# Performance work log

Hardware: AMD Instinct MI355X
Metric: run time of the kernel (lower is better)

Reference implementation:

```python
import jax, jax.numpy as jnp
import numpy as np

N_HEAD = 16
ROPE_BASE = 10000.0


def _rope_tables(T, head_dim, dtype):
    inv_freq = 1.0 / (ROPE_BASE ** (jnp.arange(0, head_dim, 2, dtype=jnp.float32) / head_dim))
    t = jnp.arange(T, dtype=jnp.float32)
    freqs = t[:, None] * inv_freq[None, :]          # [T, hd/2]
    emb = jnp.concatenate([freqs, freqs], axis=-1)  # [T, hd]
    return jnp.cos(emb).astype(dtype), jnp.sin(emb).astype(dtype)


def _rotate_half(x):
    h = x.shape[-1] // 2
    return jnp.concatenate([-x[..., h:], x[..., :h]], axis=-1)


def setup_inputs() -> dict:
    key = jax.random.key(0)
    k1, k2, k3 = jax.random.split(key, 3)
    B, T, C = 2, 2048, 1024
    x = jax.random.normal(k1, (B, T, C), dtype=jnp.float32)
    w_attn = jax.random.normal(k2, (3 * C, C), dtype=jnp.float32) * (1.0 / np.sqrt(C))
    w_proj = jax.random.normal(k3, (C, C), dtype=jnp.float32) * (1.0 / np.sqrt(C))
    return {"x": x, "w_attn": w_attn, "w_proj": w_proj}


def reference(x, w_attn, w_proj):
    B, T, C = x.shape
    H = N_HEAD
    hd = C // H

    qkv = jnp.einsum('btc,fc->btf', x, w_attn)          # [B,T,3C]
    q, k, v = jnp.split(qkv, 3, axis=-1)
    # [B,H,T,hd]
    q = q.reshape(B, T, H, hd).transpose(0, 2, 1, 3)
    k = k.reshape(B, T, H, hd).transpose(0, 2, 1, 3)
    v = v.reshape(B, T, H, hd).transpose(0, 2, 1, 3)

    cos, sin = _rope_tables(T, hd, x.dtype)             # [T,hd]
    cos = cos[None, None]
    sin = sin[None, None]
    q = q * cos + _rotate_half(q) * sin
    k = k * cos + _rotate_half(k) * sin

    scale = 1.0 / np.sqrt(hd)
    scores = jnp.einsum('bhqd,bhkd->bhqk', q, k) * scale  # [B,H,T,T]
    causal = jnp.tril(jnp.ones((T, T), dtype=bool))
    scores = jnp.where(causal[None, None], scores, jnp.finfo(scores.dtype).min)
    attn = jax.nn.softmax(scores, axis=-1)
    out = jnp.einsum('bhqk,bhkd->bhqd', attn, v)          # [B,H,T,hd]
    out = out.transpose(0, 2, 1, 3).reshape(B, T, C)
    return jnp.einsum('btc,oc->bto', out, w_proj)
```

## Files before the change

### kernel.cpp

```cpp
#include <hip/hip_runtime.h>
#include <hip/hip_bf16.h>
#include <stdint.h>

typedef unsigned short u16;
typedef __bf16 bf16x8 __attribute__((ext_vector_type(8)));
typedef float f32x4 __attribute__((ext_vector_type(4)));

#define B_ 2
#define T_ 2048
#define C_ 1024
#define H_ 16
#define HD 64
#define M_ (B_ * T_)
#define N3 (3 * C_)

#define WAITV(N) asm volatile("s_waitcnt vmcnt(" #N ")" ::: "memory")

__device__ __forceinline__ float bf2f(u16 u) {
  return __uint_as_float(((unsigned int)u) << 16);
}
__device__ __forceinline__ u16 f2bf(float f) {
  unsigned int u = __float_as_uint(f);
  u += 0x7FFF + ((u >> 16) & 1);
  return (u16)(u >> 16);
}
__device__ __forceinline__ unsigned cvt_pk_bf16(float lo, float hi) {
  unsigned r;
  asm("v_cvt_pk_bf16_f32 %0, %1, %2" : "=v"(r) : "v"(lo), "v"(hi));
  return r;
}
__device__ __forceinline__ void async16(void* ldsp, const void* gp) {
  __builtin_amdgcn_global_load_lds(
      (const __attribute__((address_space(1))) unsigned int*)gp,
      (__attribute__((address_space(3))) unsigned int*)ldsp, 16, 0, 0);
}

union U16x8 { uint4 v; u16 u[8]; };

__device__ __forceinline__ bf16x8 ldsAfrag(const char* base, int row, int kbyte) {
  int off = (row * 128 + kbyte) ^ ((row & 7) << 4);
  uint4 t = *reinterpret_cast<const uint4*>(base + off);
  return __builtin_bit_cast(bf16x8, t);
}
__device__ __forceinline__ bf16x8 ldsRead(const char* p) {
  uint4 t = *reinterpret_cast<const uint4*>(p);
  return __builtin_bit_cast(bf16x8, t);
}

#define NX4  (M_ * C_ / 4)
#define NWA4 (N3 * C_ / 4)
#define NWP4 (C_ * C_ / 4)
#define NTOT4 (NX4 + NWA4 + NWP4)
__global__ void cvt3(const float* __restrict__ x, const float* __restrict__ wa,
                     const float* __restrict__ wp, u16* __restrict__ xb,
                     u16* __restrict__ wab, u16* __restrict__ wpb) {
  int i = blockIdx.x * blockDim.x + threadIdx.x;
  int stride = gridDim.x * blockDim.x;
  for (; i < NTOT4; i += stride) {
    const float* src; u16* dst; int j = i;
    if (j < NX4) { src = x; dst = xb; }
    else if (j < NX4 + NWA4) { j -= NX4; src = wa; dst = wab; }
    else { j -= NX4 + NWA4; src = wp; dst = wpb; }
    float4 v = reinterpret_cast<const float4*>(src)[j];
    uint2 o;
    o.x = (unsigned)f2bf(v.x) | ((unsigned)f2bf(v.y) << 16);
    o.y = (unsigned)f2bf(v.z) | ((unsigned)f2bf(v.w) << 16);
    reinterpret_cast<uint2*>(dst)[j] = o;
  }
}

__global__ void rope_tables_kernel(float2* __restrict__ rtab) {
  int t = blockIdx.x;
  int i = threadIdx.x;
  float inv = powf(10000.0f, -(float)i * (1.0f / 32.0f));
  float f = (float)t * inv;
  rtab[t * 32 + i] = make_float2(cosf(f), sinf(f));
}

template <bool OUT_F32>
__global__ __launch_bounds__(256) void gemm_bt(const u16* __restrict__ A,
                                               const u16* __restrict__ Bw,
                                               void* __restrict__ Cout,
                                               int M, int N, int K) {
  __shared__ uint4 ldsbuf[2048];
  char* As = (char*)ldsbuf;
  char* Bs = (char*)ldsbuf + 16384;
  const int tid = threadIdx.x;
  const int lane = tid & 63;
  const int wv = tid >> 6;
  const int wr = wv >> 1, wc = wv & 1;
  const int lrow = lane & 15, lgrp = lane >> 4;
  const long m0 = (long)blockIdx.x * 128, n0 = (long)blockIdx.y * 128;
  const int srow_l = lane >> 3;
  const int csrc = ((lane & 7) ^ (lane >> 3)) * 8;
  f32x4 acc[4][4] = {};
  for (int k0 = 0; k0 < K; k0 += 64) {
    __syncthreads();
#pragma unroll
    for (int p = 0; p < 4; ++p) {
      int seg = wv * 4 + p;
      int row = seg * 8 + srow_l;
      async16(As + seg * 1024, A + (size_t)(m0 + row) * K + k0 + csrc);
      async16(Bs + seg * 1024, Bw + (size_t)(n0 + row) * K + k0 + csrc);
    }
    __syncthreads();
#pragma unroll
    for (int ks = 0; ks < 2; ++ks) {
      bf16x8 af[4], bfr[4];
#pragma unroll
      for (int i = 0; i < 4; ++i) {
        af[i]  = ldsAfrag(As, wr * 64 + i * 16 + lrow, ks * 64 + lgrp * 16);
        bfr[i] = ldsAfrag(Bs, wc * 64 + i * 16 + lrow, ks * 64 + lgrp * 16);
      }
#pragma unroll
      for (int i = 0; i < 4; ++i)
#pragma unroll
        for (int j = 0; j < 4; ++j)
          acc[i][j] = __builtin_amdgcn_mfma_f32_16x16x32_bf16(af[i], bfr[j], acc[i][j], 0, 0, 0);
    }
  }
#pragma unroll
  for (int i = 0; i < 4; ++i)
#pragma unroll
    for (int j = 0; j < 4; ++j) {
      long r0 = m0 + wr * 64 + i * 16 + lgrp * 4;
      long c  = n0 + wc * 64 + j * 16 + lrow;
#pragma unroll
      for (int r = 0; r < 4; ++r) {
        float v = acc[i][j][r];
        if (OUT_F32)
          ((float*)Cout)[(r0 + r) * N + c] = v;
        else
          ((u16*)Cout)[(r0 + r) * N + c] = f2bf(v);
      }
    }
}

__global__ __launch_bounds__(256) void gemm_qkv(const u16* __restrict__ A,
                                                const u16* __restrict__ Bw,
                                                const float2* __restrict__ rtab,
                                                u16* __restrict__ Qb,
                                                u16* __restrict__ Kb,
                                                u16* __restrict__ vtmp) {
  __shared__ uint4 ldsbuf[2048];
  char* As = (char*)ldsbuf;
  char* Bs = (char*)ldsbuf + 16384;
  const int tid = threadIdx.x;
  const int lane = tid & 63;
  const int wv = tid >> 6;
  const int wr = wv >> 1, wc = wv & 1;
  const int lrow = lane & 15, lgrp = lane >> 4;
  const long m0 = (long)blockIdx.x * 128, n0 = (long)blockIdx.y * 128;
  const int srow_l = lane >> 3;
  const int csrc = ((lane & 7) ^ (lane >> 3)) * 8;
  f32x4 acc[4][4] = {};
  for (int k0 = 0; k0 < C_; k0 += 64) {
    __syncthreads();
#pragma unroll
    for (int p = 0; p < 4; ++p) {
      int seg = wv * 4 + p;
      int row = seg * 8 + srow_l;
      async16(As + seg * 1024, A + (size_t)(m0 + row) * C_ + k0 + csrc);
      async16(Bs + seg * 1024, Bw + (size_t)(n0 + row) * C_ + k0 + csrc);
    }
    __syncthreads();
#pragma unroll
    for (int ks = 0; ks < 2; ++ks) {
      bf16x8 af[4], bfr[4];
#pragma unroll
      for (int i = 0; i < 4; ++i) {
        af[i]  = ldsAfrag(As, wr * 64 + i * 16 + lrow, ks * 64 + lgrp * 16);
        bfr[i] = ldsAfrag(Bs, wc * 64 + i * 16 + lrow, ks * 64 + lgrp * 16);
      }
#pragma unroll
      for (int i = 0; i < 4; ++i)
#pragma unroll
        for (int j = 0; j < 4; ++j)
          acc[i][j] = __builtin_amdgcn_mfma_f32_16x16x32_bf16(af[i], bfr[j], acc[i][j], 0, 0, 0);
    }
  }
  const float SCLQ = 0.125f * 1.4426950408889634f;
  if (n0 < 2048) {
    u16* dst = (n0 < 1024) ? Qb : Kb;
    const float scl = (n0 < 1024) ? SCLQ : 1.0f;
    const int cb = ((int)n0 & 1023) + wc * 64;
    const int h = cb >> 6;
#pragma unroll
    for (int i = 0; i < 4; ++i)
#pragma unroll
      for (int r = 0; r < 4; ++r) {
        int grow = (int)m0 + wr * 64 + i * 16 + lgrp * 4 + r;
        int b = grow >> 11, t = grow & 2047;
        const float2* rt = rtab + t * 32;
        size_t base = ((size_t)((b * 16 + h) * 2048 + t)) * 64;
#pragma unroll
        for (int j = 0; j < 2; ++j) {
          int d = j * 16 + lrow;
          float2 cn = rt[d];
          float lo = acc[i][j][r], hi = acc[i][j + 2][r];
          dst[base + d]      = f2bf((lo * cn.x - hi * cn.y) * scl);
          dst[base + d + 32] = f2bf((hi * cn.x + lo * cn.y) * scl);
        }
      }
  } else {
    const int cb = (int)n0 - 2048 + wc * 64;
#pragma unroll
    for (int i = 0; i < 4; ++i)
#pragma unroll
      for (int j = 0; j < 4; ++j) {
        int c = cb + j * 16 + lrow;
        long r0 = m0 + wr * 64 + i * 16 + lgrp * 4;
#pragma unroll
        for (int r = 0; r < 4; ++r)
          vtmp[(r0 + r) * 1024 + c] = f2bf(acc[i][j][r]);
      }
  }
}

__global__ __launch_bounds__(256) void v_transpose(const u16* __restrict__ vtmp,
                                                   u16* __restrict__ Vt) {
  __shared__ u16 Vs[64][80];
  const int tid = threadIdx.x;
  const int tblk = blockIdx.x, bh = blockIdx.y;
  const int b = bh >> 4, h = bh & 15;
  const int tl = tid >> 2, quar = tid & 3;
  const int t = tblk * 64 + tl;
  const u16* pv = vtmp + ((size_t)(b * T_ + t)) * C_ + h * HD;
#pragma unroll
  for (int c = 0; c < 2; ++c) {
    int d = quar * 16 + c * 8;
    *reinterpret_cast<uint4*>(&Vs[tl][d]) = *reinterpret_cast<const uint4*>(pv + d);
  }
  __syncthreads();
  const int d = tid >> 2, tq = tid & 3;
  U16x8 a, bv;
#pragma unroll
  for (int j = 0; j < 8; ++j) a.u[j] = Vs[tq * 16 + j][d];
#pragma unroll
  for (int j = 0; j < 8; ++j) bv.u[j] = Vs[tq * 16 + 8 + j][d];
  u16* dstv = Vt + ((size_t)bh * HD + d) * T_ + tblk * 64 + tq * 16;
  *reinterpret_cast<uint4*>(dstv) = a.v;
  *reinterpret_cast<uint4*>(dstv + 8) = bv.v;
}

__global__ __launch_bounds__(256) void attn_fwd9(const u16* __restrict__ Q,
                                                 const u16* __restrict__ K,
                                                 const u16* __restrict__ Vt,
                                                 u16* __restrict__ O) {
  __shared__ uint4 lds4[4608];
  char* ldsb = (char*)lds4;
  const int tid = threadIdx.x;
  const int lane = tid & 63, wv = tid >> 6;
  const int lrow = lane & 15, lgrp = lane >> 4;
  const int bh = blockIdx.y;
  const int b = bh >> 4, h = bh & 15;
  const u16* Qh = Q + (size_t)bh * T_ * HD;
  const u16* Kh = K + (size_t)bh * T_ * HD;
  const u16* Vh = Vt + (size_t)bh * HD * T_;

  const int srow_l = lane >> 3;
  const int csrc = ((lane & 7) ^ (lane >> 3)) * 8;

  auto stage = [&](int slot, int kt) {
    char* Kd = ldsb + (slot << 14);
    char* Vd = Kd + 8192;
    const u16* Kg = Kh + (size_t)(kt * 64) * HD;
    const u16* Vg = Vh + kt * 64;
#pragma unroll
    for (int seg = 0; seg < 2; ++seg) {
      int row = wv * 16 + seg * 8 + srow_l;
      async16(Kd + wv * 2048 + seg * 1024, Kg + (size_t)row * HD + csrc);
      async16(Vd + wv * 2048 + seg * 1024, Vg + (size_t)row * T_ + csrc);
    }
  };

  const int swz = (lrow & 7) << 4;
  const int krA = lrow * 128 + ((lgrp * 16) ^ swz);
  const int krB = lrow * 128 + ((64 + lgrp * 16) ^ swz);
  const int vrA = 8192 + krA;
  const int vrB = 8192 + krB;
  char* PsW = ldsb + 65536 + wv * 2048 + lrow * 128;
  char* pw0 = PsW + ((0 * 32 + lgrp * 8) ^ swz);
  char* pw1 = PsW + ((1 * 32 + lgrp * 8) ^ swz);
  char* pw2 = PsW + ((2 * 32 + lgrp * 8) ^ swz);
  char* pw3 = PsW + ((3 * 32 + lgrp * 8) ^ swz);
  const char* paA = PsW + ((lgrp * 16) ^ swz);
  const char* paB = PsW + ((64 + lgrp * 16) ^ swz);

  uint4 ones4;
  ones4.x = ones4.y = ones4.z = ones4.w = 0x3F803F80u;
  const bf16x8 ones8 = __builtin_bit_cast(bf16x8, ones4);

#pragma unroll
  for (int uu = 0; uu < 2; ++uu) {
    const int unit = uu ? (31 - (int)blockIdx.x) : (int)blockIdx.x;
    const int qs = unit * 64;
    const int q_glob = qs + wv * 16 + lrow;
    const int nu = unit + 1;

    bf16x8 qf[2];
#pragma unroll
    for (int ks = 0; ks < 2; ++ks) {
      uint4 t4 = *reinterpret_cast<const uint4*>(
          Qh + (size_t)(qs + wv * 16 + lrow) * HD + ks * 32 + lgrp * 8);
      qf[ks] = __builtin_bit_cast(bf16x8, t4);
    }
    f32x4 o[4] = {};
    f32x4 lacc = {};

    {
      const int pre = nu < 3 ? nu : 3;
      for (int i = 0; i < pre; ++i) stage(i, i);
      WAITV(0);
      __builtin_amdgcn_s_barrier();
      __builtin_amdgcn_sched_barrier(0);
    }

    for (int kt = 0; kt < nu; ++kt) {
      if (kt + 3 < nu) stage((kt + 3) & 3, kt + 3);
      const char* buf = ldsb + ((kt & 3) << 14);
      const char* KbA = buf + krA;
      const char* KbB = buf + krB;
      const char* VbA = buf + vrA;
      const char* VbB = buf + vrB;

      f32x4 s[4] = {};
      __builtin_amdgcn_s_setprio(1);
#pragma unroll
      for (int n = 0; n < 4; ++n)
        s[n] = __builtin_amdgcn_mfma_f32_16x16x32_bf16(ldsRead(KbA + n * 2048), qf[0], s[n], 0, 0, 0);
#pragma unroll
      for (int n = 0; n < 4; ++n)
        s[n] = __builtin_amdgcn_mfma_f32_16x16x32_bf16(ldsRead(KbB + n * 2048), qf[1], s[n], 0, 0, 0);
      __builtin_amdgcn_s_setprio(0);

      if (kt == nu - 1) {
#pragma unroll
        for (int n = 0; n < 4; ++n)
#pragma unroll
          for (int r = 0; r < 4; ++r) {
            int kg = kt * 64 + n * 16 + lgrp * 4 + r;
            float v = (kg <= q_glob) ? s[n][r] : -__builtin_inff();
            s[n][r] = exp2f(v);
          }
      } else {
#pragma unroll
        for (int n = 0; n < 4; ++n)
#pragma unroll
          for (int r = 0; r < 4; ++r) s[n][r] = exp2f(s[n][r]);
      }

      {
        uint2 w0, w1, w2, w3;
        w0.x = cvt_pk_bf16(s[0][0], s[0][1]); w0.y = cvt_pk_bf16(s[0][2], s[0][3]);
        w1.x = cvt_pk_bf16(s[1][0], s[1][1]); w1.y = cvt_pk_bf16(s[1][2], s[1][3]);
        w2.x = cvt_pk_bf16(s[2][0], s[2][1]); w2.y = cvt_pk_bf16(s[2][2], s[2][3]);
        w3.x = cvt_pk_bf16(s[3][0], s[3][1]); w3.y = cvt_pk_bf16(s[3][2], s[3][3]);
        *reinterpret_cast<uint2*>(pw0) = w0;
        *reinterpret_cast<uint2*>(pw1) = w1;
        *reinterpret_cast<uint2*>(pw2) = w2;
        *reinterpret_cast<uint2*>(pw3) = w3;
      }

      __builtin_amdgcn_s_setprio(1);
#pragma unroll
      for (int ks = 0; ks < 2; ++ks) {
        bf16x8 pa = ldsRead(ks ? paB : paA);
        lacc = __builtin_amdgcn_mfma_f32_16x16x32_bf16(pa, ones8, lacc, 0, 0, 0);
        const char* vbb = ks ? VbB : VbA;
#pragma unroll
        for (int dn = 0; dn < 4; ++dn) {
          bf16x8 bv = ldsRead(vbb + dn * 2048);
          o[dn] = __builtin_amdgcn_mfma_f32_16x16x32_bf16(pa, bv, o[dn], 0, 0, 0);
        }
      }
      __builtin_amdgcn_s_setprio(0);

      if (kt + 4 <= nu)      WAITV(8);
      else if (kt + 3 == nu) WAITV(4);
      else                   WAITV(0);
      __builtin_amdgcn_s_barrier();
      __builtin_amdgcn_sched_barrier(0);
    }

#pragma unroll
    for (int r = 0; r < 4; ++r) {
      float inv = 1.0f / lacc[r];
      int t = qs + wv * 16 + lgrp * 4 + r;
#pragma unroll
      for (int dn = 0; dn < 4; ++dn) {
        int c = h * HD + dn * 16 + lrow;
        O[((size_t)(b * T_ + t)) * C_ + c] = f2bf(o[dn][r] * inv);
      }
    }
  }
}

extern "C" void kernel_launch(void* const* d_in, const int* in_sizes, int n_in,
                              void* d_out, int out_size, void* d_ws, size_t ws_size,
                              hipStream_t stream) {
  const float* x  = (const float*)d_in[0];
  const float* wa = (const float*)d_in[1];
  const float* wp = (const float*)d_in[2];
  float* out = (float*)d_out;
  char* ws = (char*)d_ws;
  size_t off = 0;
  auto alloc = [&](size_t bytes) {
    char* p = ws + off;
    off += (bytes + 255) & ~(size_t)255;
    return p;
  };
  u16* xb   = (u16*)alloc((size_t)M_ * C_ * 2);
  u16* wab  = (u16*)alloc((size_t)N3 * C_ * 2);
  u16* wpb  = (u16*)alloc((size_t)C_ * C_ * 2);
  u16* vtmp = (u16*)alloc((size_t)M_ * C_ * 2);
  u16* Qb   = (u16*)alloc((size_t)B_ * H_ * T_ * HD * 2);
  u16* Kb   = (u16*)alloc((size_t)B_ * H_ * T_ * HD * 2);
  u16* Vtb  = (u16*)alloc((size_t)B_ * H_ * T_ * HD * 2);
  u16* Ob   = (u16*)alloc((size_t)M_ * C_ * 2);
  float2* rtab = (float2*)alloc((size_t)T_ * 32 * 8);
  (void)in_sizes; (void)n_in; (void)out_size; (void)ws_size;

  cvt3<<<2048, 256, 0, stream>>>(x, wa, wp, xb, wab, wpb);
  rope_tables_kernel<<<T_, 32, 0, stream>>>(rtab);
  gemm_qkv<<<dim3(M_ / 128, N3 / 128), 256, 0, stream>>>(xb, wab, rtab, Qb, Kb, vtmp);
  v_transpose<<<dim3(T_ / 64, B_ * H_), 256, 0, stream>>>(vtmp, Vtb);
  attn_fwd9<<<dim3(16, B_ * H_), 256, 0, stream>>>(Qb, Kb, Vtb, Ob);
  gemm_bt<true><<<dim3(M_ / 128, C_ / 128), 256, 0, stream>>>(Ob, wpb, out, M_, C_, C_);
}
```

Before: 133.6 us.

## Fuse V transpose into QKV GEMM epilogue via LDS-staged coalesced stores

The QKV GEMM epilogue now stages its output tile in LDS. Q/K rows and transposed V columns are then written to global memory with 16-byte coalesced stores. This removes the separate v_transpose kernel and the vtmp round trip through global memory, and replaces scattered 2-byte stores. It costs extra LDS (padded rows), additional barriers in the epilogue, and possible LDS bank conflicts on the transposed V writes.

```diff
diff --git a/kernel.cpp b/kernel.cpp
--- a/kernel.cpp
+++ b/kernel.cpp
@@ -141,8 +141,8 @@
                                                 const float2* __restrict__ rtab,
                                                 u16* __restrict__ Qb,
                                                 u16* __restrict__ Kb,
-                                                u16* __restrict__ vtmp) {
-  __shared__ uint4 ldsbuf[2048];
+                                                u16* __restrict__ Vt) {
+  __shared__ uint4 ldsbuf[2176];
   char* As = (char*)ldsbuf;
   char* Bs = (char*)ldsbuf + 16384;
   const int tid = threadIdx.x;
@@ -179,68 +179,61 @@
           acc[i][j] = __builtin_amdgcn_mfma_f32_16x16x32_bf16(af[i], bfr[j], acc[i][j], 0, 0, 0);
     }
   }
+
+  __syncthreads();
+  u16* ldsu = (u16*)ldsbuf;
   const float SCLQ = 0.125f * 1.4426950408889634f;
+  const int b = (int)(m0 >> 11);
+  const int t0 = (int)(m0 & 2047);
   if (n0 < 2048) {
-    u16* dst = (n0 < 1024) ? Qb : Kb;
-    const float scl = (n0 < 1024) ? SCLQ : 1.0f;
-    const int cb = ((int)n0 & 1023) + wc * 64;
-    const int h = cb >> 6;
+    const bool isq = (n0 < 1024);
+    u16* dst = isq ? Qb : Kb;
+    const float scl = isq ? SCLQ : 1.0f;
+    const int h0 = ((int)n0 & 1023) >> 6;
 #pragma unroll
     for (int i = 0; i < 4; ++i)
 #pragma unroll
       for (int r = 0; r < 4; ++r) {
-        int grow = (int)m0 + wr * 64 + i * 16 + lgrp * 4 + r;
-        int b = grow >> 11, t = grow & 2047;
-        const float2* rt = rtab + t * 32;
-        size_t base = ((size_t)((b * 16 + h) * 2048 + t)) * 64;
+        int row = wr * 64 + i * 16 + lgrp * 4 + r;
+        const float2* rt = rtab + (size_t)(t0 + row) * 32;
 #pragma unroll
         for (int j = 0; j < 2; ++j) {
-          int d = j * 16 + lrow;
-          float2 cn = rt[d];
+          int dd = j * 16 + lrow;
+          float2 cn = rt[dd];
           float lo = acc[i][j][r], hi = acc[i][j + 2][r];
-          dst[base + d]      = f2bf((lo * cn.x - hi * cn.y) * scl);
-          dst[base + d + 32] = f2bf((hi * cn.x + lo * cn.y) * scl);
+          ldsu[row * 136 + wc * 64 + dd]      = f2bf((lo * cn.x - hi * cn.y) * scl);
+          ldsu[row * 136 + wc * 64 + dd + 32] = f2bf((hi * cn.x + lo * cn.y) * scl);
         }
       }
+    __syncthreads();
+    const int row = tid >> 1, half = tid & 1;
+    const uint4* src = reinterpret_cast<const uint4*>((const char*)ldsu + row * 272 + half * 128);
+    u16* gout = dst + ((size_t)((b * 16 + h0 + half) * 2048 + t0 + row)) * 64;
+#pragma unroll
+    for (int c = 0; c < 8; ++c)
+      reinterpret_cast<uint4*>(gout)[c] = src[c];
   } else {
-    const int cb = (int)n0 - 2048 + wc * 64;
+    const int h0 = ((int)n0 - 2048) >> 6;
 #pragma unroll
     for (int i = 0; i < 4; ++i)
 #pragma unroll
       for (int j = 0; j < 4; ++j) {
-        int c = cb + j * 16 + lrow;
-        long r0 = m0 + wr * 64 + i * 16 + lgrp * 4;
-#pragma unroll
-        for (int r = 0; r < 4; ++r)
-          vtmp[(r0 + r) * 1024 + c] = f2bf(acc[i][j][r]);
-      }
+        int col = wc * 64 + j * 16 + lrow;
+#pragma unroll
+        for (int r = 0; r < 4; ++r) {
+          int row = wr * 64 + i * 16 + lgrp * 4 + r;
+          ldsu[col * 136 + row] = f2bf(acc[i][j][r]);
+        }
+      }
+    __syncthreads();
+    const int col = tid >> 1, half = tid & 1;
+    const int h = h0 + (col >> 6), dd = col & 63;
+    const uint4* src = reinterpret_cast<const uint4*>((const char*)ldsu + col * 272 + half * 128);
+    u16* gout = Vt + ((size_t)((b * 16 + h) * 64 + dd)) * 2048 + t0 + half * 64;
+#pragma unroll
+    for (int c = 0; c < 8; ++c)
+      reinterpret_cast<uint4*>(gout)[c] = src[c];
   }
-}
-
-__global__ __launch_bounds__(256) void v_transpose(const u16* __restrict__ vtmp,
-                                                   u16* __restrict__ Vt) {
-  __shared__ u16 Vs[64][80];
-  const int tid = threadIdx.x;
-  const int tblk = blockIdx.x, bh = blockIdx.y;
-  const int b = bh >> 4, h = bh & 15;
-  const int tl = tid >> 2, quar = tid & 3;
-  const int t = tblk * 64 + tl;
-  const u16* pv = vtmp + ((size_t)(b * T_ + t)) * C_ + h * HD;
-#pragma unroll
-  for (int c = 0; c < 2; ++c) {
-    int d = quar * 16 + c * 8;
-    *reinterpret_cast<uint4*>(&Vs[tl][d]) = *reinterpret_cast<const uint4*>(pv + d);
-  }
-  __syncthreads();
-  const int d = tid >> 2, tq = tid & 3;
-  U16x8 a, bv;
-#pragma unroll
-  for (int j = 0; j < 8; ++j) a.u[j] = Vs[tq * 16 + j][d];
-#pragma unroll
-  for (int j = 0; j < 8; ++j) bv.u[j] = Vs[tq * 16 + 8 + j][d];
-  u16* dstv = Vt + ((size_t)bh * HD + d) * T_ + tblk * 64 + tq * 16;
-  *reinterpret_cast<uint4*>(dstv) = a.v;
-  *reinterpret_cast<uint4*>(dstv + 8) = bv.v;
 }
 
 __global__ __launch_bounds__(256) void attn_fwd9(const u16* __restrict__ Q,
@@ -413,7 +406,6 @@
   u16* xb   = (u16*)alloc((size_t)M_ * C_ * 2);
   u16* wab  = (u16*)alloc((size_t)N3 * C_ * 2);
   u16* wpb  = (u16*)alloc((size_t)C_ * C_ * 2);
-  u16* vtmp = (u16*)alloc((size_t)M_ * C_ * 2);
   u16* Qb   = (u16*)alloc((size_t)B_ * H_ * T_ * HD * 2);
   u16* Kb   = (u16*)alloc((size_t)B_ * H_ * T_ * HD * 2);
   u16* Vtb  = (u16*)alloc((size_t)B_ * H_ * T_ * HD * 2);
@@ -423,8 +415,7 @@
 
   cvt3<<<2048, 256, 0, stream>>>(x, wa, wp, xb, wab, wpb);
   rope_tables_kernel<<<T_, 32, 0, stream>>>(rtab);
-  gemm_qkv<<<dim3(M_ / 128, N3 / 128), 256, 0, stream>>>(xb, wab, rtab, Qb, Kb, vtmp);
-  v_transpose<<<dim3(T_ / 64, B_ * H_), 256, 0, stream>>>(vtmp, Vtb);
+  gemm_qkv<<<dim3(M_ / 128, N3 / 128), 256, 0, stream>>>(xb, wab, rtab, Qb, Kb, Vtb);
   attn_fwd9<<<dim3(16, B_ * H_), 256, 0, stream>>>(Qb, Kb, Vtb, Ob);
   gemm_bt<true><<<dim3(M_ / 128, C_ / 128), 256, 0, stream>>>(Ob, wpb, out, M_, C_, C_);
 }
```

After: 134.2 us. No clear change (+0.5%).
